# Kernel optimization log

Measured on AMD Instinct MI355X. Metric: run time of the kernel, lower is better.

The kernel has to match this reference:

```python
import jax, jax.numpy as jnp
import numpy as np

IN_CH = 12      # InChannels global in original code
GROWTH = 12     # growth global == growthRate
H = 34          # peptide/pseudo-sequence length (long==34 branch)
BN_EPS = 1e-5


def setup_inputs() -> dict:
    key = jax.random.key(0)
    k = jax.random.split(key, 5)
    B, C = 16384, 72  # C = IN_CH + 5*GROWTH
    x = jax.random.normal(k[0], (B, C, H, 1), dtype=jnp.float32)
    gamma = jnp.ones((C,), dtype=jnp.float32)
    beta = jnp.zeros((C,), dtype=jnp.float32)
    conv_w = jax.random.normal(k[1], (GROWTH, C, 3, 1), dtype=jnp.float32) * 0.05
    fc_w = jax.random.normal(k[2], (1, H), dtype=jnp.float32)
    fc_bias = jax.random.normal(k[3], (1,), dtype=jnp.float32)
    return {"x": x, "gamma": gamma, "beta": beta, "conv_w": conv_w,
            "fc_w": fc_w, "fc_bias": fc_bias}


def reference(x, gamma, beta, conv_w, fc_w, fc_bias):
    B, C, Hh, Ww = x.shape
    n = (C - IN_CH) // GROWTH  # number of growth groups
    sg = jax.lax.stop_gradient

    x1 = x[:, :IN_CH]                                 # [B,12,H,1]
    x2g = x[:, IN_CH:].reshape(B, n, GROWTH, Hh, 1)    # [B,n,g,H,1]

    # per-group channel means, squeezed over the width-1 axis -> [B,n,H]
    m = x2g.mean(axis=2)[..., 0]
    x11 = x1.mean(axis=1)[..., 0]                      # [B,H]

    w = fc_w[0]                                        # [H]
    lin_m = m @ w + fc_bias[0]                         # [B,n]  (bias included per F.linear call)
    lin_out = lin_m[:, -1]                             # lin(x_outt), [B]
    lin_x11 = x11 @ w + fc_bias[0]                     # [B]

    # gate for x1: sigmoid(lin(x_outt) + lin(x11)); note bias appears twice, as in torch
    g1 = jax.nn.sigmoid(lin_out + lin_x11)             # [B]
    # gates for groups 0..n-2: sigmoid(lin(group_i) + lin(x_outt))
    gates = jax.nn.sigmoid(lin_m[:, :-1] + lin_out[:, None])  # [B,n-1]

    # the expand/repeat/view dance collapses to a per-sample scalar gate broadcast
    x1g = g1[:, None, None, None] * sg(x1)             # x1 is detached in original
    # groups are appended in reversed order (i = n-2 .. 0)
    gg = gates[:, ::-1][:, :, None, None, None] * sg(x2g[:, :-1][:, ::-1])
    gg_flat = gg.reshape(B, (n - 1) * GROWTH, Hh, 1)
    x_out = x2g[:, -1]                                 # last group, appended ungated

    xxx = jnp.concatenate([x1g, gg_flat, x_out], axis=1)  # [B,C,H,1]

    # BatchNorm2d in training mode (batch statistics, biased variance)
    mu = xxx.mean(axis=(0, 2, 3), keepdims=True)
    var = xxx.var(axis=(0, 2, 3), keepdims=True)
    xn = (xxx - mu) * jax.lax.rsqrt(var + BN_EPS)
    h = jax.nn.relu(gamma[None, :, None, None] * xn + beta[None, :, None, None])

    # Conv2d(C -> GROWTH, kernel (3,1), padding (1,0), no bias)
    out = jax.lax.conv_general_dilated(
        h, conv_w, window_strides=(1, 1), padding=((1, 1), (0, 0)),
        dimension_numbers=("NCHW", "OIHW", "NCHW"))

    return jnp.concatenate([x, out], axis=1)           # [B, C+GROWTH, H, 1]
```

## Files before the change

### kernel.cpp

```cpp
#include <hip/hip_runtime.h>
#include <hip/hip_fp16.h>
#include <math.h>


#define BN_EPS 1e-5f

#define WS_S    0
#define WS_SS   72
#define WS_A    144
#define WS_B    216
#define WS_WT   288
#define WS_GATE 3744
#define K1_BLOCKS 512

__device__ __forceinline__ float sigmoidf_(float z) { return 1.f / (1.f + expf(-z)); }

__global__ __launch_bounds__(256) void k1_stats(const float* __restrict__ x,
                                                const float* __restrict__ fw,
                                                const float* __restrict__ fb,
                                                float* __restrict__ ws,
                                                float* __restrict__ part,
                                                int B, int nTrip)
{
    __shared__ float rs_s[3][72], rss_s[3][72], wsum_s[3][72];
    __shared__ float lm_s[3][6];
    __shared__ float sc_s[3][8];
    __shared__ float Sacc[144];

    const int tid = threadIdx.x;
    const int g = tid / 72;
    const int c = tid - g * 72;
    if (tid < 144) Sacc[tid] = 0.f;

    for (int t = blockIdx.x; t < nTrip; t += K1_BLOCKS) {
        const int b0 = t * 3;

        if (tid < 216 && b0 + g < B) {
            const float2* p = (const float2*)(x + (size_t)(b0 + g) * 2448 + c * 34);
            float rs = 0.f, rss = 0.f, wsm = 0.f;
#pragma unroll
            for (int i = 0; i < 17; ++i) {
                float2 v = p[i];
                rs += v.x + v.y;
                rss = fmaf(v.x, v.x, fmaf(v.y, v.y, rss));
                wsm = fmaf(v.x, fw[2 * i], fmaf(v.y, fw[2 * i + 1], wsm));
            }
            rs_s[g][c] = rs; rss_s[g][c] = rss; wsum_s[g][c] = wsm;
        }
        __syncthreads();

        if (tid < 18) {
            int gg = tid / 6, r = tid - gg * 6;
            float s = 0.f;
#pragma unroll
            for (int k = 0; k < 12; ++k) s += wsum_s[gg][r * 12 + k];
            lm_s[gg][r] = s * (1.f / 12.f) + fb[0];
        }
        __syncthreads();

        if (tid < 3 && b0 + tid < B) {
            float lin_out = lm_s[tid][5];
            float sc[6];
            sc[0] = sigmoidf_(lin_out + lm_s[tid][0]);
            sc[1] = sigmoidf_(lm_s[tid][4] + lin_out);
            sc[2] = sigmoidf_(lm_s[tid][3] + lin_out);
            sc[3] = sigmoidf_(lm_s[tid][2] + lin_out);
            sc[4] = sigmoidf_(lm_s[tid][1] + lin_out);
            sc[5] = 1.f;
            float* gb = ws + WS_GATE + (size_t)(b0 + tid) * 6;
#pragma unroll
            for (int r = 0; r < 6; ++r) { sc_s[tid][r] = sc[r]; gb[r] = sc[r]; }
        }
        __syncthreads();

        if (tid < 72) {
            const int r = tid / 12;
            const int dd[6] = {0, 36, 12, -12, -36, 0};
            const int src = tid + dd[r];
            float a = 0.f, q = 0.f;
#pragma unroll
            for (int gg = 0; gg < 3; ++gg) {
                if (b0 + gg < B) {
                    float s = sc_s[gg][r];
                    a = fmaf(s, rs_s[gg][src], a);
                    q = fmaf(s * s, rss_s[gg][src], q);
                }
            }
            Sacc[tid] += a; Sacc[72 + tid] += q;
        }
        __syncthreads();
    }

    if (tid < 144) part[(size_t)tid * K1_BLOCKS + blockIdx.x] = Sacc[tid];
}

__global__ __launch_bounds__(256) void k2a_reduce(float* __restrict__ ws,
                                                  const float* __restrict__ part)
{
    const int ch = blockIdx.x;
    const float* p = part + (size_t)ch * K1_BLOCKS;
    float s = 0.f;
    for (int i = threadIdx.x; i < K1_BLOCKS; i += 256) s += p[i];
#pragma unroll
    for (int off = 32; off; off >>= 1) s += __shfl_down(s, off, 64);
    __shared__ float wsum[4];
    if ((threadIdx.x & 63) == 0) wsum[threadIdx.x >> 6] = s;
    __syncthreads();
    if (threadIdx.x == 0) ws[WS_S + ch] = wsum[0] + wsum[1] + wsum[2] + wsum[3];
}

__global__ void k2b_finalize(const float* __restrict__ gamma,
                             const float* __restrict__ beta,
                             const float* __restrict__ cw,
                             float* __restrict__ ws, float invN)
{
    const int tid = threadIdx.x;
    if (tid < 72) {
        float S = ws[WS_S + tid], SS = ws[WS_SS + tid];
        float mu = S * invN;
        float var = SS * invN - mu * mu;
        float inv = rsqrtf(var + BN_EPS);
        float A = gamma[tid] * inv;
        ws[WS_A + tid] = A;
        ws[WS_B + tid] = beta[tid] - mu * A;
    }
    for (int i = tid; i < 12 * 72 * 3; i += 256) {
        int o = i / 216, rem = i - o * 216;
        int c = rem / 3, k = rem - c * 3;
        ws[WS_WT + c * 48 + o * 4 + k] = cw[i];
    }
}

__global__ __launch_bounds__(256) void k3_out(const float* __restrict__ x,
                                              const float* __restrict__ ws,
                                              float* __restrict__ out, int B)
{
    __shared__ __align__(16) __half hs[6 * 2456];
    __shared__ float2 AB[73];
    __shared__ float gl[6][8];

    const int tid = threadIdx.x;
    const int b0 = blockIdx.x * 6;
    int nb = B - b0; if (nb > 6) nb = 6;

    if (tid < 73)
        AB[tid] = (tid < 72) ? make_float2(ws[WS_A + tid], ws[WS_B + tid])
                             : make_float2(0.f, 0.f);
    for (int t2 = tid; t2 < nb * 6; t2 += 256) {
        int g = t2 / 6, j = t2 - g * 6;
        gl[g][j] = ws[WS_GATE + (size_t)(b0 + g) * 6 + j];
    }
    if (tid < 24) {
        int g = tid >> 2, k = tid & 3;
        ((unsigned int*)hs)[g * 1228 + ((k < 2) ? k : (1224 + k))] = 0u;
    }
    __syncthreads();

    for (int idx = tid; idx < nb * 612; idx += 256) {
        int g = idx / 612, v4 = idx - g * 612;
        size_t b = (size_t)(b0 + g);
        float4 q = ((const float4*)(x + b * 2448))[v4];
        ((float4*)(out + b * 2856))[v4] = q;

        const int ddc[6]  = {0, 36, 12, -12, -36, 0};
        const int sidx[6] = {0, 4, 3, 2, 1, 5};
        int rx = v4 / 102;
        int e  = v4 * 4;
        int cx0 = e / 34;
        int h0i = e - cx0 * 34;
        int dd  = ddc[rx];
        int cd0 = cx0 + dd;
        float2 ab0 = AB[cd0];
        float2 ab1 = AB[cd0 + 1];
        float s = gl[g][sidx[rx]];
        float vv[4] = {q.x, q.y, q.z, q.w};
        __half hv[4];
#pragma unroll
        for (int j = 0; j < 4; ++j) {
            float2 ab = (h0i + j >= 34) ? ab1 : ab0;
            hv[j] = __float2half(fmaxf(fmaf(ab.x * s, vv[j], ab.y), 0.f));
        }
        union { __half2 h2; unsigned int u; } pa, pb;
        pa.h2 = __halves2half2(hv[0], hv[1]);
        pb.h2 = __halves2half2(hv[2], hv[3]);
        int dst = g * 2456 + 4 + e + dd * 34;
        *reinterpret_cast<uint2*>(&hs[dst]) = make_uint2(pa.u, pb.u);
    }
    __syncthreads();

    const float4* wT = (const float4*)(ws + WS_WT);
    for (int it = tid; it < nb * 34; it += 256) {
        int g = it / 34, hh = it - g * 34;
        const __half* hb = &hs[g * 2456 + 4 + hh];
        float m0 = (hh == 0) ? 0.f : 1.f;
        float m2 = (hh == 33) ? 0.f : 1.f;
        float acc[12];
#pragma unroll
        for (int o = 0; o < 12; ++o) acc[o] = 0.f;
        for (int c = 0; c < 72; ++c) {
            float h0 = m0 * __half2float(hb[c * 34 - 1]);
            float h1 =      __half2float(hb[c * 34]);
            float h2 = m2 * __half2float(hb[c * 34 + 1]);
#pragma unroll
            for (int o = 0; o < 12; ++o) {
                float4 wv = wT[c * 12 + o];
                acc[o] = fmaf(h0, wv.x, fmaf(h1, wv.y, fmaf(h2, wv.z, acc[o])));
            }
        }
        float* op = out + (size_t)(b0 + g) * 2856 + 2448;
#pragma unroll
        for (int o = 0; o < 12; ++o) op[o * 34 + hh] = acc[o];
    }
}

extern "C" void kernel_launch(void* const* d_in, const int* in_sizes, int n_in,
                              void* d_out, int out_size, void* d_ws, size_t ws_size,
                              hipStream_t stream)
{
    const float* x     = (const float*)d_in[0];
    const float* gamma = (const float*)d_in[1];
    const float* beta  = (const float*)d_in[2];
    const float* cw    = (const float*)d_in[3];
    const float* fw    = (const float*)d_in[4];
    const float* fb    = (const float*)d_in[5];
    float* out = (float*)d_out;
    float* ws  = (float*)d_ws;

    const int B = in_sizes[0] / (72 * 34);
    const int nTrip = (B + 2) / 3;
    float* part = ws + WS_GATE + (size_t)B * 6;

    k1_stats<<<K1_BLOCKS, 256, 0, stream>>>(x, fw, fb, ws, part, B, nTrip);
    k2a_reduce<<<144, 256, 0, stream>>>(ws, part);
    k2b_finalize<<<1, 256, 0, stream>>>(gamma, beta, cw, ws, 1.f / ((float)B * 34.f));
    k3_out<<<(B + 5) / 6, 256, 0, stream>>>(x, ws, out, B);
}
```

Before: 399.5 us.

## Compute the 3-tap conv in k3 with MFMA f16 instead of scalar FMAs

The finalize kernel now stores the conv weights as fp16 MFMA A-fragments (three shifts by three K-slices, padded to 16 outputs and 96 channels). k3_out loads these into registers and computes the (3,1) convolution with mfma_f32_16x16x32_f16 over 16-column tiles of the fp16 LDS activations, plus a tail tile for columns 32-33. Boundary padding is handled by extra MFMAs that subtract the wrapped-in neighbour values. This removes the scalar per-thread FMA loop, whose fp32 weight reads dominated the conv stage. In exchange it adds strided 16-bit LDS gathers to build B fragments and more complex masking logic.

```diff
diff --git a/kernel.cpp b/kernel.cpp
--- a/kernel.cpp
+++ b/kernel.cpp
@@ -12,6 +12,9 @@
 #define WS_WT   288
 #define WS_GATE 3744
 #define K1_BLOCKS 512
+
+typedef _Float16 f16x8 __attribute__((ext_vector_type(8)));
+typedef float f32x4 __attribute__((ext_vector_type(4)));
 
 __device__ __forceinline__ float sigmoidf_(float z) { return 1.f / (1.f + expf(-z)); }
 
@@ -124,10 +127,16 @@
         ws[WS_A + tid] = A;
         ws[WS_B + tid] = beta[tid] - mu * A;
     }
-    for (int i = tid; i < 12 * 72 * 3; i += 256) {
-        int o = i / 216, rem = i - o * 216;
-        int c = rem / 3, k = rem - c * 3;
-        ws[WS_WT + c * 48 + o * 4 + k] = cw[i];
+    __half* wa = (__half*)(ws + WS_WT);
+    for (int i = tid; i < 9 * 64 * 8; i += 256) {
+        int j = i & 7;
+        int lane = (i >> 3) & 63;
+        int frag = i >> 9;
+        int shift = frag / 3, ks = frag - shift * 3;
+        int o = lane & 15, grp = lane >> 4;
+        int ct = ks * 32 + grp * 8 + j;
+        float v = (o < 12 && ct < 72) ? cw[o * 216 + ct * 3 + shift] : 0.f;
+        wa[i] = __float2half(v);
     }
 }
 
@@ -140,8 +149,16 @@
     __shared__ float gl[6][8];
 
     const int tid = threadIdx.x;
+    const int lane = tid & 63;
+    const int wid = tid >> 6;
     const int b0 = blockIdx.x * 6;
     int nb = B - b0; if (nb > 6) nb = 6;
+
+    const __half* wa = (const __half*)(ws + WS_WT);
+    f16x8 wA[9];
+#pragma unroll
+    for (int f = 0; f < 9; ++f)
+        wA[f] = *(const f16x8*)(wa + (f * 64 + lane) * 8);
 
     if (tid < 73)
         AB[tid] = (tid < 72) ? make_float2(ws[WS_A + tid], ws[WS_B + tid])
@@ -153,6 +170,10 @@
     if (tid < 24) {
         int g = tid >> 2, k = tid & 3;
         ((unsigned int*)hs)[g * 1228 + ((k < 2) ? k : (1224 + k))] = 0u;
+    }
+    if (nb < 6) {
+        for (int i = tid; i < (6 - nb) * 1228; i += 256)
+            ((unsigned int*)hs)[nb * 1228 + i] = 0u;
     }
     __syncthreads();
 
@@ -188,28 +209,65 @@
     }
     __syncthreads();
 
-    const float4* wT = (const float4*)(ws + WS_WT);
-    for (int it = tid; it < nb * 34; it += 256) {
-        int g = it / 34, hh = it - g * 34;
-        const __half* hb = &hs[g * 2456 + 4 + hh];
-        float m0 = (hh == 0) ? 0.f : 1.f;
-        float m2 = (hh == 33) ? 0.f : 1.f;
-        float acc[12];
-#pragma unroll
-        for (int o = 0; o < 12; ++o) acc[o] = 0.f;
-        for (int c = 0; c < 72; ++c) {
-            float h0 = m0 * __half2float(hb[c * 34 - 1]);
-            float h1 =      __half2float(hb[c * 34]);
-            float h2 = m2 * __half2float(hb[c * 34 + 1]);
-#pragma unroll
-            for (int o = 0; o < 12; ++o) {
-                float4 wv = wT[c * 12 + o];
-                acc[o] = fmaf(h0, wv.x, fmaf(h1, wv.y, fmaf(h2, wv.z, acc[o])));
-            }
-        }
-        float* op = out + (size_t)(b0 + g) * 2856 + 2448;
-#pragma unroll
-        for (int o = 0; o < 12; ++o) op[o * 34 + hh] = acc[o];
+    const int sub = lane & 15, grp = lane >> 4;
+    for (int t = wid; t < 13; t += 4) {
+        const bool tail = (t == 12);
+        int g, col;
+        if (!tail) { g = t >> 1; col = (t & 1) * 16 + sub; }
+        else       { g = (sub < 12) ? (sub >> 1) : 0; col = 32 + (sub & 1); }
+        if (!tail && g >= nb) continue;
+
+        const __half* hb = &hs[g * 2456 + 4];
+        f32x4 acc = {0.f, 0.f, 0.f, 0.f};
+        f16x8 save0, save1, save2;
+        const bool needc = tail || ((t & 1) == 0);
+        const int  csh   = tail ? 2 : 0;
+
+#pragma unroll
+        for (int ks = 0; ks < 3; ++ks) {
+            const int cb = (ks < 2) ? (ks * 32 + grp * 8) : 64;
+            const __half* hc = hb + cb * 34 + col;
+#pragma unroll
+            for (int sh = 0; sh < 3; ++sh) {
+                f16x8 bf;
+#pragma unroll
+                for (int j = 0; j < 8; ++j)
+                    ((unsigned short*)&bf)[j] =
+                        *(const unsigned short*)(hc + j * 34 + (sh - 1));
+                if (needc && sh == csh) {
+                    if (ks == 0) save0 = bf;
+                    else if (ks == 1) save1 = bf;
+                    else save2 = bf;
+                }
+                acc = __builtin_amdgcn_mfma_f32_16x16x32_f16(
+                          wA[sh * 3 + ks], bf, acc, 0, 0, 0);
+            }
+        }
+
+        if (needc) {
+            const bool m = tail ? (((sub & 1) == 1) && sub < 12) : (sub == 0);
+#pragma unroll
+            for (int ks = 0; ks < 3; ++ks) {
+                const f16x8& sv = (ks == 0) ? save0 : (ks == 1) ? save1 : save2;
+                f16x8 bt;
+#pragma unroll
+                for (int w = 0; w < 4; ++w)
+                    ((unsigned int*)&bt)[w] =
+                        m ? (((const unsigned int*)&sv)[w] ^ 0x80008000u) : 0u;
+                acc = __builtin_amdgcn_mfma_f32_16x16x32_f16(
+                          wA[csh * 3 + ks], bt, acc, 0, 0, 0);
+            }
+        }
+
+        const bool gok = tail ? (sub < 12 && g < nb) : true;
+        if (gok) {
+            float* op = out + (size_t)(b0 + g) * 2856 + 2448 + col;
+#pragma unroll
+            for (int j = 0; j < 4; ++j) {
+                int o = grp * 4 + j;
+                if (o < 12) op[o * 34] = acc[j];
+            }
+        }
     }
 }
 
```

After: 387.3 us. -3.1%, faster.
